# Kernel tuning notes

Measured on AMD Instinct MI355X. Metric: run time of the kernel, lower is better.

## Reference

```python
import jax, jax.numpy as jnp
import numpy as np

D_IN = 1024
D_OUT = 1024

def setup_inputs() -> dict:
    key = jax.random.key(0)
    kx, kq, kk, kv = jax.random.split(key, 4)
    scale = 1.0 / np.sqrt(D_IN)
    return {
        "x": jax.random.normal(kx, (4, 4096, D_IN), dtype=jnp.float32),
        "W_q": jax.random.uniform(kq, (D_IN, D_OUT), dtype=jnp.float32, minval=-scale, maxval=scale),
        "W_k": jax.random.uniform(kk, (D_IN, D_OUT), dtype=jnp.float32, minval=-scale, maxval=scale),
        "W_v": jax.random.uniform(kv, (D_IN, D_OUT), dtype=jnp.float32, minval=-scale, maxval=scale),
    }

def reference(x, W_q, W_k, W_v):
    # x: [b, s, d_in]; weights stored as [d_in, d_out] (transposed vs torch Linear)
    Q = jnp.einsum('bsd,de->bse', x, W_q)
    K = jnp.einsum('bsd,de->bse', x, W_k)
    V = jnp.einsum('bsd,de->bse', x, W_v)
    d_k = K.shape[-1]
    scores = jnp.einsum('bqe,bke->bqk', Q, K) / jnp.sqrt(jnp.asarray(d_k, x.dtype))
    weights = jax.nn.softmax(scores, axis=-1)
    return jnp.einsum('bqk,bke->bqe', weights, V)
```

## Files before the change

### kernel.cpp

```cpp
#include <hip/hip_runtime.h>

typedef unsigned short u16;
typedef float f32x4 __attribute__((ext_vector_type(4)));
typedef u16   u16x4 __attribute__((ext_vector_type(4)));
typedef u16   u16x8 __attribute__((ext_vector_type(8)));
typedef __bf16 bf16x8 __attribute__((ext_vector_type(8)));

static __device__ __forceinline__ u16 f2bf(float x) {
    unsigned int u = __builtin_bit_cast(unsigned int, x);
    u = (u + 0x7FFFu + ((u >> 16) & 1u)) >> 16;
    return (u16)u;
}
static __device__ __forceinline__ float bf2f(u16 x) {
    unsigned int u = ((unsigned int)x) << 16;
    return __builtin_bit_cast(float, u);
}
static __device__ __forceinline__ bf16x8 as_bf(u16x8 v) { return __builtin_bit_cast(bf16x8, v); }

static __device__ __forceinline__ void gload16(const u16* g, u16* lds) {
    __builtin_amdgcn_global_load_lds(
        (const __attribute__((address_space(1))) void*)g,
        (__attribute__((address_space(3))) void*)lds,
        16, 0, 0);
}

#define KSCALE 0.045084220027780106f

#define STAGE_G2L(dst, src, stride, ROUNDS) do {                               \
    _Pragma("unroll") for (int i_ = 0; i_ < (ROUNDS); ++i_) {                  \
        int c_ = (i_ * 4 + w) * 64 + l;                                        \
        int row_ = c_ >> 3, c8_ = c_ & 7;                                      \
        gload16((src) + (size_t)row_ * (stride) + ((c8_ ^ (row_ & 7)) << 3),   \
                &(dst)[(i_ * 4 + w) * 512]);                                   \
    } } while (0)

__global__ __launch_bounds__(256) void wt_kernel(const float* __restrict__ Wq,
                                                 const float* __restrict__ Wk,
                                                 const float* __restrict__ Wv,
                                                 u16* __restrict__ Wt) {
    __shared__ float tile[64][65];
    const int mat = blockIdx.z;
    const float* W = (mat == 0) ? Wq : ((mat == 1) ? Wk : Wv);
    const int bx = blockIdx.x, by = blockIdx.y;
    const int tid = threadIdx.x;
#pragma unroll
    for (int i = 0; i < 16; ++i) {
        int idx = i * 256 + tid;
        int r = idx >> 6, c = idx & 63;
        tile[r][c] = W[(by * 64 + r) * 1024 + bx * 64 + c];
    }
    __syncthreads();
#pragma unroll
    for (int i = 0; i < 16; ++i) {
        int idx = i * 256 + tid;
        int r = idx >> 6, c = idx & 63;
        Wt[mat * 1048576 + (bx * 64 + r) * 1024 + by * 64 + c] = f2bf(tile[c][r]);
    }
}

__global__ __launch_bounds__(256, 3) void qkv_gemm(const float* __restrict__ X,
                                                   const u16* __restrict__ Wt,
                                                   u16* __restrict__ Qo,
                                                   u16* __restrict__ Ko,
                                                   u16* __restrict__ Vt) {
    __shared__ u16 As[128 * 64];
    __shared__ u16 Bs[128 * 64];
    const int bid = blockIdx.x;
    const int swz = (bid & 7) * 96 + (bid >> 3);
    const int bm = swz / 24, bn = swz % 24;
    const int tid = threadIdx.x;
    const int w = tid >> 6, l = tid & 63, lg = l >> 4, lr = l & 15;
    const int wr = w >> 1, wc = w & 1;

    const f32x4 z4 = {0.f, 0.f, 0.f, 0.f};
    f32x4 acc[4][4];
#pragma unroll
    for (int m = 0; m < 4; ++m)
#pragma unroll
        for (int n = 0; n < 4; ++n) acc[m][n] = z4;

    for (int kb = 0; kb < 16; ++kb) {
        __syncthreads();
        STAGE_G2L(Bs, Wt + (size_t)(bn * 128) * 1024 + kb * 64, 1024, 4);
#pragma unroll
        for (int i = 0; i < 4; ++i) {
            int cid = i * 256 + tid;
            int row = cid >> 3, c8 = cid & 7;
            const float* src = X + (bm * 128 + row) * 1024 + kb * 64 + c8 * 8;
            f32x4 v0 = *(const f32x4*)(src);
            f32x4 v1 = *(const f32x4*)(src + 4);
            u16x8 t;
            t[0] = f2bf(v0[0]); t[1] = f2bf(v0[1]); t[2] = f2bf(v0[2]); t[3] = f2bf(v0[3]);
            t[4] = f2bf(v1[0]); t[5] = f2bf(v1[1]); t[6] = f2bf(v1[2]); t[7] = f2bf(v1[3]);
            *(u16x8*)(&As[row * 64 + ((c8 ^ (row & 7)) << 3)]) = t;
        }
        __syncthreads();
#pragma unroll
        for (int kk = 0; kk < 2; ++kk) {
            bf16x8 af[4], bfr[4];
#pragma unroll
            for (int m = 0; m < 4; ++m) {
                int row = wr * 64 + m * 16 + lr;
                af[m] = as_bf(*(const u16x8*)(&As[row * 64 + (((kk * 4 + lg) ^ (lr & 7)) << 3)]));
            }
#pragma unroll
            for (int n = 0; n < 4; ++n) {
                int row = wc * 64 + n * 16 + lr;
                bfr[n] = as_bf(*(const u16x8*)(&Bs[row * 64 + (((kk * 4 + lg) ^ (lr & 7)) << 3)]));
            }
#pragma unroll
            for (int m = 0; m < 4; ++m)
#pragma unroll
                for (int n = 0; n < 4; ++n)
                    acc[m][n] = __builtin_amdgcn_mfma_f32_16x16x32_bf16(af[m], bfr[n], acc[m][n], 0, 0, 0);
        }
    }
    const int row0 = bm * 128 + wr * 64;
    const int col0 = bn * 128 + wc * 64;
#pragma unroll
    for (int m = 0; m < 4; ++m) {
#pragma unroll
        for (int n = 0; n < 4; ++n) {
            int col = col0 + n * 16 + lr;
            int mat = col >> 10;
            int cg = col & 1023;
            int row = row0 + m * 16 + lg * 4;
            if (mat == 2) {
                u16x4 v;
                v[0] = f2bf(acc[m][n][0]); v[1] = f2bf(acc[m][n][1]);
                v[2] = f2bf(acc[m][n][2]); v[3] = f2bf(acc[m][n][3]);
                *(u16x4*)(Vt + cg * 4096 + row) = v;
            } else {
                u16* P = mat ? Ko : Qo;
#pragma unroll
                for (int r = 0; r < 4; ++r) P[(row + r) * 1024 + cg] = f2bf(acc[m][n][r]);
            }
        }
    }
}

template <bool WRITE_PL>
__global__ __launch_bounds__(256, 4) void qk_gemm(const u16* __restrict__ Qb,
                                                  const u16* __restrict__ Kb,
                                                  u16* __restrict__ P,
                                                  float* __restrict__ pl) {
    __shared__ u16 As[128 * 64];
    __shared__ u16 Bs[128 * 64];
    const int bid = blockIdx.x;
    const int swz = (bid & 7) * 128 + (bid >> 3);
    const int bm = swz >> 5, bn = swz & 31;
    const int tid = threadIdx.x;
    const int w = tid >> 6, l = tid & 63, lg = l >> 4, lr = l & 15;
    const int wr = w >> 1, wc = w & 1;

    const f32x4 z4 = {0.f, 0.f, 0.f, 0.f};
    f32x4 acc[4][4];
#pragma unroll
    for (int m = 0; m < 4; ++m)
#pragma unroll
        for (int n = 0; n < 4; ++n) acc[m][n] = z4;

    for (int kb = 0; kb < 16; ++kb) {
        __syncthreads();
        STAGE_G2L(As, Qb + (size_t)(bm * 128) * 1024 + kb * 64, 1024, 4);
        STAGE_G2L(Bs, Kb + (size_t)(bn * 128) * 1024 + kb * 64, 1024, 4);
        __syncthreads();
#pragma unroll
        for (int kk = 0; kk < 2; ++kk) {
            bf16x8 af[4], bfr[4];
#pragma unroll
            for (int m = 0; m < 4; ++m) {
                int row = wr * 64 + m * 16 + lr;
                af[m] = as_bf(*(const u16x8*)(&As[row * 64 + (((kk * 4 + lg) ^ (lr & 7)) << 3)]));
            }
#pragma unroll
            for (int n = 0; n < 4; ++n) {
                int row = wc * 64 + n * 16 + lr;
                bfr[n] = as_bf(*(const u16x8*)(&Bs[row * 64 + (((kk * 4 + lg) ^ (lr & 7)) << 3)]));
            }
#pragma unroll
            for (int m = 0; m < 4; ++m)
#pragma unroll
                for (int n = 0; n < 4; ++n)
                    acc[m][n] = __builtin_amdgcn_mfma_f32_16x16x32_bf16(af[m], bfr[n], acc[m][n], 0, 0, 0);
        }
    }
    const int row0 = bm * 128 + wr * 64;
    const int col0 = bn * 128 + wc * 64;
#pragma unroll
    for (int m = 0; m < 4; ++m) {
#pragma unroll
        for (int r = 0; r < 4; ++r) {
            const size_t rowg = (size_t)(row0 + m * 16 + lg * 4 + r);
            float se = 0.f;
#pragma unroll
            for (int n = 0; n < 4; ++n) {
                u16 pb = f2bf(exp2f(acc[m][n][r] * KSCALE));
                P[rowg * 4096 + col0 + n * 16 + lr] = pb;
                if (WRITE_PL) se += bf2f(pb);
            }
            if (WRITE_PL) {
                se += __shfl_xor(se, 1, 64);
                se += __shfl_xor(se, 2, 64);
                se += __shfl_xor(se, 4, 64);
                se += __shfl_xor(se, 8, 64);
                if (lr == 0) pl[rowg * 64 + bn * 2 + wc] = se;
            }
        }
    }
}

__global__ __launch_bounds__(256) void rowsum_pair(const u16* __restrict__ P0,
                                                   const u16* __restrict__ P1,
                                                   float* __restrict__ rlb) {
    const int gw = blockIdx.x * 4 + (threadIdx.x >> 6);
    const int l = threadIdx.x & 63;
    const u16* P = (gw < 4096) ? P0 : P1;
    const u16* pr = P + (size_t)(gw & 4095) * 4096 + l * 8;
    float s = 0.f;
#pragma unroll
    for (int j = 0; j < 8; ++j) {
        u16x8 v = *(const u16x8*)(pr + j * 512);
#pragma unroll
        for (int e = 0; e < 8; ++e) s += bf2f(v[e]);
    }
    s += __shfl_xor(s, 1, 64);
    s += __shfl_xor(s, 2, 64);
    s += __shfl_xor(s, 4, 64);
    s += __shfl_xor(s, 8, 64);
    s += __shfl_xor(s, 16, 64);
    s += __shfl_xor(s, 32, 64);
    if (l == 0) rlb[gw] = 1.0f / s;
}

template <int MODE>
__global__ __launch_bounds__(256, 4) void pv_pair(const u16* __restrict__ P0,
                                                  const u16* __restrict__ P1,
                                                  const u16* __restrict__ V0,
                                                  const u16* __restrict__ V1,
                                                  const float* __restrict__ pl,
                                                  float* __restrict__ Out0,
                                                  float* __restrict__ Out1) {
    __shared__ u16 As[128 * 64];
    __shared__ u16 Bs[128 * 64];
    __shared__ float rl_s[128];
    const int bid = blockIdx.x;
    const int swz = (bid & 7) * 64 + (bid >> 3);
    const int bb = swz >> 8, rem = swz & 255;
    const int bm = rem >> 3, bn = rem & 7;
    const int q0 = bm * 128, e0 = bn * 128;
    const u16* P  = bb ? P1 : P0;
    const u16* Vt = bb ? V1 : V0;
    float* Out    = bb ? Out1 : Out0;
    const int tid = threadIdx.x;
    const int w = tid >> 6, l = tid & 63, lg = l >> 4, lr = l & 15;
    const int wr = w >> 1, wc = w & 1;

    if (MODE == 0) {
        if (tid < 128) {
            const f32x4* pp = (const f32x4*)(pl + (size_t)(bb * 4096 + q0 + tid) * 64);
            f32x4 a = pp[0];
#pragma unroll
            for (int i = 1; i < 16; ++i) a += pp[i];
            rl_s[tid] = 1.0f / (a[0] + a[1] + a[2] + a[3]);
        }
    } else {
        if (tid < 128) rl_s[tid] = pl[bb * 4096 + q0 + tid];
    }

    const f32x4 z4 = {0.f, 0.f, 0.f, 0.f};
    f32x4 acc[4][4];
#pragma unroll
    for (int m = 0; m < 4; ++m)
#pragma unroll
        for (int n = 0; n < 4; ++n) acc[m][n] = z4;

    for (int kb = 0; kb < 64; ++kb) {
        __syncthreads();
        STAGE_G2L(As, P + (size_t)q0 * 4096 + kb * 64, 4096, 4);
        STAGE_G2L(Bs, Vt + (size_t)e0 * 4096 + kb * 64, 4096, 4);
        __syncthreads();
#pragma unroll
        for (int kk = 0; kk < 2; ++kk) {
            bf16x8 af[4], bfr[4];
#pragma unroll
            for (int m = 0; m < 4; ++m) {
                int row = wr * 64 + m * 16 + lr;
                af[m] = as_bf(*(const u16x8*)(&As[row * 64 + (((kk * 4 + lg) ^ (lr & 7)) << 3)]));
            }
#pragma unroll
            for (int n = 0; n < 4; ++n) {
                int row = wc * 64 + n * 16 + lr;
                bfr[n] = as_bf(*(const u16x8*)(&Bs[row * 64 + (((kk * 4 + lg) ^ (lr & 7)) << 3)]));
            }
#pragma unroll
            for (int m = 0; m < 4; ++m)
#pragma unroll
                for (int n = 0; n < 4; ++n)
                    acc[m][n] = __builtin_amdgcn_mfma_f32_16x16x32_bf16(af[m], bfr[n], acc[m][n], 0, 0, 0);
        }
    }
#pragma unroll
    for (int m = 0; m < 4; ++m) {
#pragma unroll
        for (int r = 0; r < 4; ++r) {
            int rloc = wr * 64 + m * 16 + lg * 4 + r;
            float rl = rl_s[rloc];
#pragma unroll
            for (int n = 0; n < 4; ++n)
                Out[(size_t)(q0 + rloc) * 1024 + e0 + wc * 64 + n * 16 + lr] = acc[m][n][r] * rl;
        }
    }
}

extern "C" void kernel_launch(void* const* d_in, const int* in_sizes, int n_in,
                              void* d_out, int out_size, void* d_ws, size_t ws_size,
                              hipStream_t stream) {
    const float* x  = (const float*)d_in[0];
    const float* Wq = (const float*)d_in[1];
    const float* Wk = (const float*)d_in[2];
    const float* Wv = (const float*)d_in[3];
    float* out = (float*)d_out;

    char* ws = (char*)d_ws;
    u16* Wt = (u16*)(ws);
    u16* Qb = (u16*)(ws + 6291456);
    u16* Kb = (u16*)(ws + 14680064);
    u16* V0 = (u16*)(ws + 23068672);
    u16* V1 = (u16*)(ws + 31457280);
    u16* P0 = (u16*)(ws + 39845888);
    u16* P1 = (u16*)(ws + 73400320);
    float* plg = (float*)(ws + 106954752);
    float* rlb = (float*)Qb;

    const bool big = (ws_size >= 106954752u + 2097152u);

    wt_kernel<<<dim3(16, 16, 3), 256, 0, stream>>>(Wq, Wk, Wv, Wt);
    for (int p = 0; p < 2; ++p) {
        const float* x0 = x + (size_t)(2 * p) * 4194304;
        const float* x1 = x + (size_t)(2 * p + 1) * 4194304;
        float* o0 = out + (size_t)(2 * p) * 4194304;
        float* o1 = out + (size_t)(2 * p + 1) * 4194304;
        qkv_gemm<<<dim3(768), 256, 0, stream>>>(x0, Wt, Qb, Kb, V0);
        if (big) qk_gemm<true><<<dim3(1024), 256, 0, stream>>>(Qb, Kb, P0, plg);
        else     qk_gemm<false><<<dim3(1024), 256, 0, stream>>>(Qb, Kb, P0, nullptr);
        qkv_gemm<<<dim3(768), 256, 0, stream>>>(x1, Wt, Qb, Kb, V1);
        if (big) qk_gemm<true><<<dim3(1024), 256, 0, stream>>>(Qb, Kb, P1, plg + 4096 * 64);
        else     qk_gemm<false><<<dim3(1024), 256, 0, stream>>>(Qb, Kb, P1, nullptr);
        if (big) {
            pv_pair<0><<<dim3(512), 256, 0, stream>>>(P0, P1, V0, V1, plg, o0, o1);
        } else {
            rowsum_pair<<<dim3(2048), 256, 0, stream>>>(P0, P1, rlb);
            pv_pair<1><<<dim3(512), 256, 0, stream>>>(P0, P1, V0, V1, rlb, o0, o1);
        }
    }
}
```

Before: 452.6 us.

## Reassociate QK^T as x(WqWk^T)x^T to drop the separate Q and K projections

Precomputes G = Wq·Wk^T once, then computes Y = x·G alongside V in a single fused GEMM. Scores are formed as Y·x^T, with x converted from fp32 to bf16 on the fly inside the score kernel. This removes one of the three projection GEMMs per batch and the K intermediate buffer. The score kernel now reads fp32 x, which doubles its B-operand traffic, and it runs at lower occupancy. The extra bf16 rounding of G and Y may change accuracy. The small-workspace rowsum fallback is also removed.

```diff
diff --git a/kernel.cpp b/kernel.cpp
--- a/kernel.cpp
+++ b/kernel.cpp
@@ -34,40 +34,48 @@
                 &(dst)[(i_ * 4 + w) * 512]);                                   \
     } } while (0)
 
-__global__ __launch_bounds__(256) void wt_kernel(const float* __restrict__ Wq,
-                                                 const float* __restrict__ Wk,
-                                                 const float* __restrict__ Wv,
-                                                 u16* __restrict__ Wt) {
+#define STAGE_F2B(dst, src, stride) do {                                       \
+    _Pragma("unroll") for (int i_ = 0; i_ < 4; ++i_) {                         \
+        int cid_ = i_ * 256 + tid;                                             \
+        int row_ = cid_ >> 3, c8_ = cid_ & 7;                                  \
+        const float* s_ = (src) + (size_t)row_ * (stride) + c8_ * 8;           \
+        f32x4 v0_ = *(const f32x4*)(s_);                                       \
+        f32x4 v1_ = *(const f32x4*)(s_ + 4);                                   \
+        u16x8 t_;                                                              \
+        t_[0] = f2bf(v0_[0]); t_[1] = f2bf(v0_[1]);                            \
+        t_[2] = f2bf(v0_[2]); t_[3] = f2bf(v0_[3]);                            \
+        t_[4] = f2bf(v1_[0]); t_[5] = f2bf(v1_[1]);                            \
+        t_[6] = f2bf(v1_[2]); t_[7] = f2bf(v1_[3]);                            \
+        *(u16x8*)(&(dst)[row_ * 64 + ((c8_ ^ (row_ & 7)) << 3)]) = t_;         \
+    } } while (0)
+
+__global__ __launch_bounds__(256) void wt_kernel(const float* __restrict__ Wv,
+                                                 u16* __restrict__ Wvt) {
     __shared__ float tile[64][65];
-    const int mat = blockIdx.z;
-    const float* W = (mat == 0) ? Wq : ((mat == 1) ? Wk : Wv);
     const int bx = blockIdx.x, by = blockIdx.y;
     const int tid = threadIdx.x;
 #pragma unroll
     for (int i = 0; i < 16; ++i) {
         int idx = i * 256 + tid;
         int r = idx >> 6, c = idx & 63;
-        tile[r][c] = W[(by * 64 + r) * 1024 + bx * 64 + c];
+        tile[r][c] = Wv[(by * 64 + r) * 1024 + bx * 64 + c];
     }
     __syncthreads();
 #pragma unroll
     for (int i = 0; i < 16; ++i) {
         int idx = i * 256 + tid;
         int r = idx >> 6, c = idx & 63;
-        Wt[mat * 1048576 + (bx * 64 + r) * 1024 + by * 64 + c] = f2bf(tile[c][r]);
-    }
-}
-
-__global__ __launch_bounds__(256, 3) void qkv_gemm(const float* __restrict__ X,
-                                                   const u16* __restrict__ Wt,
-                                                   u16* __restrict__ Qo,
-                                                   u16* __restrict__ Ko,
-                                                   u16* __restrict__ Vt) {
+        Wvt[(bx * 64 + r) * 1024 + by * 64 + c] = f2bf(tile[c][r]);
+    }
+}
+
+__global__ __launch_bounds__(256, 3) void g_gemm(const float* __restrict__ Wk,
+                                                 const float* __restrict__ Wq,
+                                                 u16* __restrict__ Gt) {
     __shared__ u16 As[128 * 64];
     __shared__ u16 Bs[128 * 64];
     const int bid = blockIdx.x;
-    const int swz = (bid & 7) * 96 + (bid >> 3);
-    const int bm = swz / 24, bn = swz % 24;
+    const int bm = bid >> 3, bn = bid & 7;
     const int tid = threadIdx.x;
     const int w = tid >> 6, l = tid & 63, lg = l >> 4, lr = l & 15;
     const int wr = w >> 1, wc = w & 1;
@@ -81,19 +89,8 @@
 
     for (int kb = 0; kb < 16; ++kb) {
         __syncthreads();
-        STAGE_G2L(Bs, Wt + (size_t)(bn * 128) * 1024 + kb * 64, 1024, 4);
-#pragma unroll
-        for (int i = 0; i < 4; ++i) {
-            int cid = i * 256 + tid;
-            int row = cid >> 3, c8 = cid & 7;
-            const float* src = X + (bm * 128 + row) * 1024 + kb * 64 + c8 * 8;
-            f32x4 v0 = *(const f32x4*)(src);
-            f32x4 v1 = *(const f32x4*)(src + 4);
-            u16x8 t;
-            t[0] = f2bf(v0[0]); t[1] = f2bf(v0[1]); t[2] = f2bf(v0[2]); t[3] = f2bf(v0[3]);
-            t[4] = f2bf(v1[0]); t[5] = f2bf(v1[1]); t[6] = f2bf(v1[2]); t[7] = f2bf(v1[3]);
-            *(u16x8*)(&As[row * 64 + ((c8 ^ (row & 7)) << 3)]) = t;
-        }
+        STAGE_F2B(As, Wk + (size_t)(bm * 128) * 1024 + kb * 64, 1024);
+        STAGE_F2B(Bs, Wq + (size_t)(bn * 128) * 1024 + kb * 64, 1024);
         __syncthreads();
 #pragma unroll
         for (int kk = 0; kk < 2; ++kk) {
@@ -118,30 +115,88 @@
     const int row0 = bm * 128 + wr * 64;
     const int col0 = bn * 128 + wc * 64;
 #pragma unroll
+    for (int m = 0; m < 4; ++m)
+#pragma unroll
+        for (int n = 0; n < 4; ++n)
+#pragma unroll
+            for (int r = 0; r < 4; ++r)
+                Gt[(size_t)(row0 + m * 16 + lg * 4 + r) * 1024 + col0 + n * 16 + lr]
+                    = f2bf(acc[m][n][r]);
+}
+
+__global__ __launch_bounds__(256, 3) void yv_gemm(const float* __restrict__ X,
+                                                  const u16* __restrict__ Gt,
+                                                  const u16* __restrict__ Wvt,
+                                                  u16* __restrict__ Y,
+                                                  u16* __restrict__ Vt) {
+    __shared__ u16 As[128 * 64];
+    __shared__ u16 Bs[128 * 64];
+    const int bid = blockIdx.x;
+    const int swz = (bid & 7) * 64 + (bid >> 3);
+    const int bm = swz >> 4, bn = swz & 15;
+    const int tid = threadIdx.x;
+    const int w = tid >> 6, l = tid & 63, lg = l >> 4, lr = l & 15;
+    const int wr = w >> 1, wc = w & 1;
+
+    const u16* bsrc = (bn < 8) ? (Gt  + (size_t)(bn * 128) * 1024)
+                               : (Wvt + (size_t)((bn - 8) * 128) * 1024);
+
+    const f32x4 z4 = {0.f, 0.f, 0.f, 0.f};
+    f32x4 acc[4][4];
+#pragma unroll
+    for (int m = 0; m < 4; ++m)
+#pragma unroll
+        for (int n = 0; n < 4; ++n) acc[m][n] = z4;
+
+    for (int kb = 0; kb < 16; ++kb) {
+        __syncthreads();
+        STAGE_G2L(Bs, bsrc + kb * 64, 1024, 4);
+        STAGE_F2B(As, X + (size_t)(bm * 128) * 1024 + kb * 64, 1024);
+        __syncthreads();
+#pragma unroll
+        for (int kk = 0; kk < 2; ++kk) {
+            bf16x8 af[4], bfr[4];
+#pragma unroll
+            for (int m = 0; m < 4; ++m) {
+                int row = wr * 64 + m * 16 + lr;
+                af[m] = as_bf(*(const u16x8*)(&As[row * 64 + (((kk * 4 + lg) ^ (lr & 7)) << 3)]));
+            }
+#pragma unroll
+            for (int n = 0; n < 4; ++n) {
+                int row = wc * 64 + n * 16 + lr;
+                bfr[n] = as_bf(*(const u16x8*)(&Bs[row * 64 + (((kk * 4 + lg) ^ (lr & 7)) << 3)]));
+            }
+#pragma unroll
+            for (int m = 0; m < 4; ++m)
+#pragma unroll
+                for (int n = 0; n < 4; ++n)
+                    acc[m][n] = __builtin_amdgcn_mfma_f32_16x16x32_bf16(af[m], bfr[n], acc[m][n], 0, 0, 0);
+        }
+    }
+    const int row0 = bm * 128 + wr * 64;
+    const int col0 = bn * 128 + wc * 64;
+#pragma unroll
     for (int m = 0; m < 4; ++m) {
 #pragma unroll
         for (int n = 0; n < 4; ++n) {
             int col = col0 + n * 16 + lr;
-            int mat = col >> 10;
-            int cg = col & 1023;
             int row = row0 + m * 16 + lg * 4;
-            if (mat == 2) {
+            if (bn < 8) {
+#pragma unroll
+                for (int r = 0; r < 4; ++r) Y[(size_t)(row + r) * 1024 + col] = f2bf(acc[m][n][r]);
+            } else {
+                int cg = col & 1023;
                 u16x4 v;
                 v[0] = f2bf(acc[m][n][0]); v[1] = f2bf(acc[m][n][1]);
                 v[2] = f2bf(acc[m][n][2]); v[3] = f2bf(acc[m][n][3]);
-                *(u16x4*)(Vt + cg * 4096 + row) = v;
-            } else {
-                u16* P = mat ? Ko : Qo;
-#pragma unroll
-                for (int r = 0; r < 4; ++r) P[(row + r) * 1024 + cg] = f2bf(acc[m][n][r]);
-            }
-        }
-    }
-}
-
-template <bool WRITE_PL>
-__global__ __launch_bounds__(256, 4) void qk_gemm(const u16* __restrict__ Qb,
-                                                  const u16* __restrict__ Kb,
+                *(u16x4*)(Vt + (size_t)cg * 4096 + row) = v;
+            }
+        }
+    }
+}
+
+__global__ __launch_bounds__(256, 3) void qk_gemm(const u16* __restrict__ Yb,
+                                                  const float* __restrict__ Xf,
                                                   u16* __restrict__ P,
                                                   float* __restrict__ pl) {
     __shared__ u16 As[128 * 64];
@@ -162,8 +217,8 @@
 
     for (int kb = 0; kb < 16; ++kb) {
         __syncthreads();
-        STAGE_G2L(As, Qb + (size_t)(bm * 128) * 1024 + kb * 64, 1024, 4);
-        STAGE_G2L(Bs, Kb + (size_t)(bn * 128) * 1024 + kb * 64, 1024, 4);
+        STAGE_G2L(As, Yb + (size_t)(bm * 128) * 1024 + kb * 64, 1024, 4);
+        STAGE_F2B(Bs, Xf + (size_t)(bn * 128) * 1024 + kb * 64, 1024);
         __syncthreads();
 #pragma unroll
         for (int kk = 0; kk < 2; ++kk) {
@@ -197,43 +252,17 @@
             for (int n = 0; n < 4; ++n) {
                 u16 pb = f2bf(exp2f(acc[m][n][r] * KSCALE));
                 P[rowg * 4096 + col0 + n * 16 + lr] = pb;
-                if (WRITE_PL) se += bf2f(pb);
-            }
-            if (WRITE_PL) {
-                se += __shfl_xor(se, 1, 64);
-                se += __shfl_xor(se, 2, 64);
-                se += __shfl_xor(se, 4, 64);
-                se += __shfl_xor(se, 8, 64);
-                if (lr == 0) pl[rowg * 64 + bn * 2 + wc] = se;
-            }
-        }
-    }
-}
-
-__global__ __launch_bounds__(256) void rowsum_pair(const u16* __restrict__ P0,
-                                                   const u16* __restrict__ P1,
-                                                   float* __restrict__ rlb) {
-    const int gw = blockIdx.x * 4 + (threadIdx.x >> 6);
-    const int l = threadIdx.x & 63;
-    const u16* P = (gw < 4096) ? P0 : P1;
-    const u16* pr = P + (size_t)(gw & 4095) * 4096 + l * 8;
-    float s = 0.f;
-#pragma unroll
-    for (int j = 0; j < 8; ++j) {
-        u16x8 v = *(const u16x8*)(pr + j * 512);
-#pragma unroll
-        for (int e = 0; e < 8; ++e) s += bf2f(v[e]);
-    }
-    s += __shfl_xor(s, 1, 64);
-    s += __shfl_xor(s, 2, 64);
-    s += __shfl_xor(s, 4, 64);
-    s += __shfl_xor(s, 8, 64);
-    s += __shfl_xor(s, 16, 64);
-    s += __shfl_xor(s, 32, 64);
-    if (l == 0) rlb[gw] = 1.0f / s;
-}
-
-template <int MODE>
+                se += bf2f(pb);
+            }
+            se += __shfl_xor(se, 1, 64);
+            se += __shfl_xor(se, 2, 64);
+            se += __shfl_xor(se, 4, 64);
+            se += __shfl_xor(se, 8, 64);
+            if (lr == 0) pl[rowg * 64 + bn * 2 + wc] = se;
+        }
+    }
+}
+
 __global__ __launch_bounds__(256, 4) void pv_pair(const u16* __restrict__ P0,
                                                   const u16* __restrict__ P1,
                                                   const u16* __restrict__ V0,
@@ -256,16 +285,12 @@
     const int w = tid >> 6, l = tid & 63, lg = l >> 4, lr = l & 15;
     const int wr = w >> 1, wc = w & 1;
 
-    if (MODE == 0) {
-        if (tid < 128) {
-            const f32x4* pp = (const f32x4*)(pl + (size_t)(bb * 4096 + q0 + tid) * 64);
-            f32x4 a = pp[0];
-#pragma unroll
-            for (int i = 1; i < 16; ++i) a += pp[i];
-            rl_s[tid] = 1.0f / (a[0] + a[1] + a[2] + a[3]);
-        }
-    } else {
-        if (tid < 128) rl_s[tid] = pl[bb * 4096 + q0 + tid];
+    if (tid < 128) {
+        const f32x4* pp = (const f32x4*)(pl + (size_t)(bb * 4096 + q0 + tid) * 64);
+        f32x4 a = pp[0];
+#pragma unroll
+        for (int i = 1; i < 16; ++i) a += pp[i];
+        rl_s[tid] = 1.0f / (a[0] + a[1] + a[2] + a[3]);
     }
 
     const f32x4 z4 = {0.f, 0.f, 0.f, 0.f};
@@ -323,35 +348,26 @@
     float* out = (float*)d_out;
 
     char* ws = (char*)d_ws;
-    u16* Wt = (u16*)(ws);
-    u16* Qb = (u16*)(ws + 6291456);
-    u16* Kb = (u16*)(ws + 14680064);
-    u16* V0 = (u16*)(ws + 23068672);
-    u16* V1 = (u16*)(ws + 31457280);
-    u16* P0 = (u16*)(ws + 39845888);
-    u16* P1 = (u16*)(ws + 73400320);
-    float* plg = (float*)(ws + 106954752);
-    float* rlb = (float*)Qb;
-
-    const bool big = (ws_size >= 106954752u + 2097152u);
-
-    wt_kernel<<<dim3(16, 16, 3), 256, 0, stream>>>(Wq, Wk, Wv, Wt);
+    u16*   Gt  = (u16*)(ws);
+    u16*   Wvt = (u16*)(ws + 2097152);
+    float* plg = (float*)(ws + 4194304);
+    u16*   Y   = (u16*)(ws + 6291456);
+    u16*   V0  = (u16*)(ws + 14680064);
+    u16*   V1  = (u16*)(ws + 23068672);
+    u16*   P0  = (u16*)(ws + 31457280);
+    u16*   P1  = (u16*)(ws + 65011712);
+
+    wt_kernel<<<dim3(16, 16), 256, 0, stream>>>(Wv, Wvt);
+    g_gemm<<<dim3(64), 256, 0, stream>>>(Wk, Wq, Gt);
     for (int p = 0; p < 2; ++p) {
         const float* x0 = x + (size_t)(2 * p) * 4194304;
         const float* x1 = x + (size_t)(2 * p + 1) * 4194304;
         float* o0 = out + (size_t)(2 * p) * 4194304;
         float* o1 = out + (size_t)(2 * p + 1) * 4194304;
-        qkv_gemm<<<dim3(768), 256, 0, stream>>>(x0, Wt, Qb, Kb, V0);
-        if (big) qk_gemm<true><<<dim3(1024), 256, 0, stream>>>(Qb, Kb, P0, plg);
-        else     qk_gemm<false><<<dim3(1024), 256, 0, stream>>>(Qb, Kb, P0, nullptr);
-        qkv_gemm<<<dim3(768), 256, 0, stream>>>(x1, Wt, Qb, Kb, V1);
-        if (big) qk_gemm<true><<<dim3(1024), 256, 0, stream>>>(Qb, Kb, P1, plg + 4096 * 64);
-        else     qk_gemm<false><<<dim3(1024), 256, 0, stream>>>(Qb, Kb, P1, nullptr);
-        if (big) {
-            pv_pair<0><<<dim3(512), 256, 0, stream>>>(P0, P1, V0, V1, plg, o0, o1);
-        } else {
-            rowsum_pair<<<dim3(2048), 256, 0, stream>>>(P0, P1, rlb);
-            pv_pair<1><<<dim3(512), 256, 0, stream>>>(P0, P1, V0, V1, rlb, o0, o1);
-        }
-    }
-}
+        yv_gemm<<<dim3(512), 256, 0, stream>>>(x0, Gt, Wvt, Y, V0);
+        qk_gemm<<<dim3(1024), 256, 0, stream>>>(Y, x0, P0, plg);
+        yv_gemm<<<dim3(512), 256, 0, stream>>>(x1, Gt, Wvt, Y, V1);
+        qk_gemm<<<dim3(1024), 256, 0, stream>>>(Y, x1, P1, plg + 262144);
+        pv_pair<<<dim3(512), 256, 0, stream>>>(P0, P1, V0, V1, plg, o0, o1);
+    }
+}
```

After: 595.9 us. 1.32x slower.
